# Kernel optimization log

Measured on AMD Instinct MI355X. Metric: run time of the kernel, lower is better.

The kernel has to match this reference:

```python
import jax, jax.numpy as jnp
import numpy as np

T, D, I, E, G, LG, K = 2048, 1024, 512, 32, 8, 4, 6
SI = 2 * I  # shared expert inter dim = n_shared_experts * inter_dim
ROUTE_SCALE = 1.0


def setup_inputs() -> dict:
    key = jax.random.key(0)
    ks = jax.random.split(key, 16)
    s = 0.02
    f = jnp.float32
    return {
        "x": jax.random.normal(ks[0], (T, D), f),
        "router_w": jax.random.normal(ks[1], (E, D), f) * s,
        "router_b": jax.random.normal(ks[2], (E,), f) * s,
        "W1": jax.random.normal(ks[3], (E, D, I), f) * s,
        "b1": jax.random.normal(ks[4], (E, I), f) * s,
        "W2": jax.random.normal(ks[5], (E, D, I), f) * s,
        "b2": jax.random.normal(ks[6], (E, I), f) * s,
        "W3": jax.random.normal(ks[7], (E, I, D), f) * s,
        "b3": jax.random.normal(ks[8], (E, D), f) * s,
        "sw1": jax.random.normal(ks[9], (D, SI), f) * s,
        "sb1": jax.random.normal(ks[10], (SI,), f) * s,
        "sw2": jax.random.normal(ks[11], (D, SI), f) * s,
        "sb2": jax.random.normal(ks[12], (SI,), f) * s,
        "sw3": jax.random.normal(ks[13], (SI, D), f) * s,
        "sb3": jax.random.normal(ks[14], (D,), f) * s,
    }


def _route(x, router_w, router_b):
    # Router: softmax scores (fp32), group-limited top-k.
    logits = x @ router_w.T + router_b                      # [T, E]
    scores = jax.nn.softmax(logits.astype(jnp.float32), axis=-1)
    original = scores
    sg = scores.reshape(x.shape[0], G, E // G)              # [T, G, E/G]
    # no router bias -> group score = sum of top-2 expert scores per group
    group_scores = jnp.sum(jax.lax.top_k(sg, 2)[0], axis=-1)  # [T, G]
    _, gidx = jax.lax.top_k(group_scores, LG)               # [T, LG]
    keep = jnp.zeros((x.shape[0], G), bool).at[jnp.arange(x.shape[0])[:, None], gidx].set(True)
    masked = jnp.where(keep[:, :, None], sg, -jnp.inf).reshape(x.shape[0], E)
    _, idx = jax.lax.top_k(masked, K)                       # [T, K]
    vals = jnp.take_along_axis(original, idx, axis=1) * ROUTE_SCALE
    return vals.astype(x.dtype), idx


def reference(x, router_w, router_b, W1, b1, W2, b2, W3, b3, sw1, sb1, sw2, sb2, sw3, sb3):
    vals, idx = _route(x, router_w, router_b)
    # dense gate matrix [T, E]; top-k indices per row are distinct
    gates = jnp.zeros((x.shape[0], E), x.dtype).at[jnp.arange(x.shape[0])[:, None], idx].set(vals)
    # routed experts: Expert(x) = W3 @ silu(w1(x) * w2(x))
    h1 = jnp.einsum('td,edi->tei', x, W1) + b1              # [T, E, I]
    h2 = jnp.einsum('td,edi->tei', x, W2) + b2
    h = jax.nn.silu(h1 * h2)
    y = jnp.einsum('tei,eid->td', h * gates[:, :, None], W3) + gates @ b3
    # shared expert
    z = jax.nn.silu((x @ sw1 + sb1) * (x @ sw2 + sb2)) @ sw3 + sb3
    return y + z
```

## Files before the change

### kernel.cpp

```cpp
#include <hip/hip_runtime.h>
#include <hip/hip_bf16.h>
#include <math.h>

#define T_CONST 2048
#define D_CONST 1024
#define I_CONST 512
#define SI_CONST 1024
#define E_CONST 32
#define G_CONST 8
#define LG_CONST 4
#define KSEL 6

#define BM 128
#define BN 64
#define BK 64

typedef __attribute__((ext_vector_type(8))) short short8;
typedef __attribute__((ext_vector_type(4))) float floatx4;

__device__ inline unsigned pack_bf16(float a, float b) {
  __hip_bfloat162 h = __float22bfloat162_rn(float2{a, b});
  return *reinterpret_cast<unsigned*>(&h);
}

__device__ inline void gload16(const void* g, void* l) {
  __builtin_amdgcn_global_load_lds(
      (const __attribute__((address_space(1))) unsigned int*)g,
      (__attribute__((address_space(3))) unsigned int*)l, 16, 0, 0);
}

__global__ __launch_bounds__(256) void cvt_x(const float* __restrict__ in,
                                             __hip_bfloat16* __restrict__ out) {
  size_t i = ((size_t)blockIdx.x * 256 + threadIdx.x) * 4;
  float4 v = *(const float4*)&in[i];
  uint2 u{pack_bf16(v.x, v.y), pack_bf16(v.z, v.w)};
  *(uint2*)&out[i] = u;
}

__global__ __launch_bounds__(256) void cvt_rwt(const float* __restrict__ rw,
                                               float* __restrict__ rwt) {
  int i = blockIdx.x * 256 + threadIdx.x;
  int d = i >> 5, e = i & 31;
  rwt[d * 32 + e] = rw[e * D_CONST + d];
}

__global__ __launch_bounds__(256) void transpose_all(
    const float* __restrict__ W1, const float* __restrict__ W2,
    const float* __restrict__ W3, const float* __restrict__ sw1,
    const float* __restrict__ sw2, const float* __restrict__ sw3,
    __hip_bfloat16* __restrict__ W1t, __hip_bfloat16* __restrict__ W2t,
    __hip_bfloat16* __restrict__ W3t, __hip_bfloat16* __restrict__ sw1t,
    __hip_bfloat16* __restrict__ sw2t, __hip_bfloat16* __restrict__ sw3t) {
  __shared__ float tile[64][65];
  int b = blockIdx.x;
  const float* in;
  __hip_bfloat16* out;
  int K, N, k0, n0;
  if (b < 8192) {
    int local = b & 4095;
    int mat = local >> 7, rem = local & 127;
    K = 1024; N = 512;
    in = ((b < 4096) ? W1 : W2) + (size_t)mat * (1024 * 512);
    out = ((b < 4096) ? W1t : W2t) + (size_t)mat * (1024 * 512);
    n0 = (rem & 7) * 64; k0 = (rem >> 3) * 64;
  } else if (b < 12288) {
    int local = b - 8192;
    int mat = local >> 7, rem = local & 127;
    K = 512; N = 1024;
    in = W3 + (size_t)mat * (512 * 1024);
    out = W3t + (size_t)mat * (512 * 1024);
    n0 = (rem & 15) * 64; k0 = (rem >> 4) * 64;
  } else {
    int local = b - 12288;
    int which = local >> 8, rem = local & 255;
    K = 1024; N = 1024;
    in = which == 0 ? sw1 : which == 1 ? sw2 : sw3;
    out = which == 0 ? sw1t : which == 1 ? sw2t : sw3t;
    n0 = (rem & 15) * 64; k0 = (rem >> 4) * 64;
  }
  int tid = threadIdx.x;
  int tr = tid >> 4, tc4 = (tid & 15) * 4;
#pragma unroll
  for (int i = 0; i < 4; ++i) {
    float4 v = *(const float4*)&in[(size_t)(k0 + tr + 16 * i) * N + n0 + tc4];
    tile[tr + 16 * i][tc4 + 0] = v.x;
    tile[tr + 16 * i][tc4 + 1] = v.y;
    tile[tr + 16 * i][tc4 + 2] = v.z;
    tile[tr + 16 * i][tc4 + 3] = v.w;
  }
  __syncthreads();
#pragma unroll
  for (int i = 0; i < 4; ++i) {
    int n = tr + 16 * i;
    unsigned lo = pack_bf16(tile[tc4 + 0][n], tile[tc4 + 1][n]);
    unsigned hi = pack_bf16(tile[tc4 + 2][n], tile[tc4 + 3][n]);
    uint2 u{lo, hi};
    *(uint2*)&out[(size_t)(n0 + n) * K + k0 + tc4] = u;
  }
}

__global__ __launch_bounds__(256) void router2(
    const float* __restrict__ x, const float* __restrict__ rwt,
    const float* __restrict__ rb, int* __restrict__ counts,
    int* __restrict__ slots, float* __restrict__ gatel) {
  const int lane = threadIdx.x & 63;
  const int wv = threadIdx.x >> 6;
  const int t = blockIdx.x * 4 + wv;
  const int e = lane & 31, h = lane >> 5;
  const float* xp = x + (size_t)t * D_CONST;
  float s = 0.f;
#pragma unroll 8
  for (int d = h; d < D_CONST; d += 2) s = fmaf(xp[d], rwt[d * 32 + e], s);
  s += __shfl_xor(s, 32);
  s += rb[e];
  float mx = s;
#pragma unroll
  for (int m = 16; m >= 1; m >>= 1) mx = fmaxf(mx, __shfl_xor(mx, m));
  float p = expf(s - mx);
  float sum = p;
#pragma unroll
  for (int m = 16; m >= 1; m >>= 1) sum += __shfl_xor(sum, m);
  float sc = p / sum;
  float a = sc, bb = __shfl_xor(a, 1);
  float hi = fmaxf(a, bb), lo = fminf(a, bb);
  float oh = __shfl_xor(hi, 2), ol = __shfl_xor(lo, 2);
  float gs = fmaxf(fmaxf(hi + oh, hi + lo), oh + ol);
  const int g = e >> 2;
  unsigned keep = 0;
  float gv = gs;
#pragma unroll
  for (int r = 0; r < LG_CONST; ++r) {
    float v = gv;
    int gi = g;
#pragma unroll
    for (int m = 16; m >= 1; m >>= 1) {
      float ov = __shfl_xor(v, m);
      int og = __shfl_xor(gi, m);
      if (ov > v || (ov == v && og < gi)) { v = ov; gi = og; }
    }
    keep |= 1u << gi;
    if (g == gi) gv = -1e30f;
  }
  float cand = ((keep >> g) & 1u) ? sc : -1e30f;
  int sel_e = -1;
  float sel_v = 0.f;
#pragma unroll
  for (int r = 0; r < KSEL; ++r) {
    float v = cand;
    int ei = e;
#pragma unroll
    for (int m = 16; m >= 1; m >>= 1) {
      float ov = __shfl_xor(v, m);
      int oe = __shfl_xor(ei, m);
      if (ov > v || (ov == v && oe < ei)) { v = ov; ei = oe; }
    }
    if (lane == r) { sel_e = ei; sel_v = v; }
    if (e == ei) cand = -1e30f;
  }
  if (lane < KSEL) {
    int pos = atomicAdd(&counts[sel_e], 1);
    slots[sel_e * T_CONST + pos] = t * KSEL + lane;
    gatel[sel_e * T_CONST + pos] = sel_v;
  }
}

template <bool GATHER>
__global__ __launch_bounds__(256, 2) void up_mfma2(
    const __hip_bfloat16* __restrict__ Abf, const __hip_bfloat16* __restrict__ B1t,
    const __hip_bfloat16* __restrict__ B2t, const float* __restrict__ bias1,
    const float* __restrict__ bias2, const int* __restrict__ counts,
    const int* __restrict__ slots, __hip_bfloat16* __restrict__ Hout,
    int N, int Kd) {
  const int e = GATHER ? blockIdx.z : 0;
  const int cnt = GATHER ? counts[e] : T_CONST;
  const int m0 = blockIdx.y * BM;
  if (m0 >= cnt) return;
  const int n0 = blockIdx.x * BN;

  __shared__ short As[8 * BM * 8];
  __shared__ short Bs1[8 * BN * 8];
  __shared__ short Bs2[8 * BN * 8];
  __shared__ int srow[BM];
  __shared__ int sdst[BM];

  const int tid = threadIdx.x;
  const int lane = tid & 63, wv = tid >> 6;
  if (tid < BM) {
    int r = m0 + tid;
    bool valid = r < cnt;
    if (GATHER) {
      int sl = valid ? slots[e * T_CONST + r] : 0;
      srow[tid] = valid ? sl / KSEL : 0;
      sdst[tid] = valid ? sl : -1;
    } else {
      srow[tid] = valid ? r : 0;
      sdst[tid] = valid ? r : -1;
    }
  }
  __syncthreads();

  const char* agp[4];
  short* alds[4];
  const char* bgp[4];
  short* blds[4];
  {
    int row0 = srow[lane], row1 = srow[64 + lane];
#pragma unroll
    for (int i = 0; i < 4; ++i) {
      int kc = 2 * wv + (i >> 1);
      int mh = i & 1;
      agp[i] = (const char*)(Abf + (size_t)(mh ? row1 : row0) * Kd + kc * 8);
      alds[i] = (short*)As + (kc * BM + mh * 64 + lane) * 8;
    }
    const __hip_bfloat16* Bsel = (wv < 2 ? B1t : B2t) + (size_t)e * N * Kd;
    short* Lsel = (wv < 2) ? (short*)Bs1 : (short*)Bs2;
    int wl = wv & 1;
#pragma unroll
    for (int i = 0; i < 4; ++i) {
      int kc = wl * 4 + i;
      bgp[i] = (const char*)(Bsel + (size_t)(n0 + lane) * Kd + kc * 8);
      blds[i] = Lsel + (kc * BN + lane) * 8;
    }
  }

  const int l15 = lane & 15, quad = lane >> 4;
  const int wm = wv & 1, wn = wv >> 1;
  floatx4 acc1[4][2] = {};
  floatx4 acc2[4][2] = {};
  const int kiter = Kd / BK;

  for (int it = 0; it < kiter; ++it) {
#pragma unroll
    for (int i = 0; i < 4; ++i) gload16(agp[i], alds[i]);
#pragma unroll
    for (int i = 0; i < 4; ++i) gload16(bgp[i], blds[i]);
#pragma unroll
    for (int i = 0; i < 4; ++i) { agp[i] += BK * 2; bgp[i] += BK * 2; }
    __syncthreads();
    short8 a[2][4];
#pragma unroll
    for (int s = 0; s < 2; ++s)
#pragma unroll
      for (int mi = 0; mi < 4; ++mi)
        a[s][mi] = *(const short8*)&As[((s * 4 + quad) * BM + wm * 64 + mi * 16 + l15) * 8];
#pragma unroll
    for (int s = 0; s < 2; ++s)
#pragma unroll
      for (int ni = 0; ni < 2; ++ni) {
        short8 b1 = *(const short8*)&Bs1[((s * 4 + quad) * BN + wn * 32 + ni * 16 + l15) * 8];
        short8 b2 = *(const short8*)&Bs2[((s * 4 + quad) * BN + wn * 32 + ni * 16 + l15) * 8];
#pragma unroll
        for (int mi = 0; mi < 4; ++mi) {
          acc1[mi][ni] = __builtin_amdgcn_mfma_f32_16x16x32_bf16(a[s][mi], b1, acc1[mi][ni], 0, 0, 0);
          acc2[mi][ni] = __builtin_amdgcn_mfma_f32_16x16x32_bf16(a[s][mi], b2, acc2[mi][ni], 0, 0, 0);
        }
      }
    __syncthreads();
  }

  const float* bb1 = bias1 + (size_t)e * N + n0;
  const float* bb2 = bias2 + (size_t)e * N + n0;
#pragma unroll
  for (int mi = 0; mi < 4; ++mi) {
#pragma unroll
    for (int ni = 0; ni < 2; ++ni) {
      int n = wn * 32 + ni * 16 + l15;
      float c1 = bb1[n], c2 = bb2[n];
#pragma unroll
      for (int reg = 0; reg < 4; ++reg) {
        int row = wm * 64 + mi * 16 + quad * 4 + reg;
        int dst = sdst[row];
        if (dst < 0) continue;
        float h1 = acc1[mi][ni][reg] + c1;
        float h2 = acc2[mi][ni][reg] + c2;
        float p = h1 * h2;
        float sv = p / (1.f + expf(-p));
        Hout[(size_t)dst * N + n0 + n] = __float2bfloat16(sv);
      }
    }
  }
}

template <bool ROUTED>
__global__ __launch_bounds__(256, 2) void down_mfma2(
    const __hip_bfloat16* __restrict__ Hin, const __hip_bfloat16* __restrict__ Bt,
    const float* __restrict__ bd, const int* __restrict__ counts,
    const int* __restrict__ slots, const float* __restrict__ gatel,
    float* __restrict__ Out, int Kd) {
  const int e = ROUTED ? blockIdx.z : 0;
  const int cnt = ROUTED ? counts[e] : T_CONST;
  const int m0 = blockIdx.y * BM;
  if (m0 >= cnt) return;
  const int n0 = blockIdx.x * BN;

  __shared__ short As[8 * BM * 8];
  __shared__ short Bs[8 * BN * 8];
  __shared__ int ssrc[BM];
  __shared__ int stok[BM];
  __shared__ float sg[BM];

  const int tid = threadIdx.x;
  const int lane = tid & 63, wv = tid >> 6;
  if (tid < BM) {
    int r = m0 + tid;
    bool valid = r < cnt;
    if (ROUTED) {
      int sl = valid ? slots[e * T_CONST + r] : 0;
      ssrc[tid] = sl;
      stok[tid] = valid ? (sl / KSEL) : -1;
      sg[tid] = valid ? gatel[e * T_CONST + r] : 0.f;
    } else {
      ssrc[tid] = valid ? r : 0;
      stok[tid] = valid ? r : -1;
      sg[tid] = 1.f;
    }
  }
  __syncthreads();

  const char* agp[4];
  short* alds[4];
  const char* bgp[2];
  short* blds[2];
  {
    int row0 = ssrc[lane], row1 = ssrc[64 + lane];
#pragma unroll
    for (int i = 0; i < 4; ++i) {
      int kc = 2 * wv + (i >> 1);
      int mh = i & 1;
      agp[i] = (const char*)(Hin + (size_t)(mh ? row1 : row0) * Kd + kc * 8);
      alds[i] = (short*)As + (kc * BM + mh * 64 + lane) * 8;
    }
    const __hip_bfloat16* Bsel = Bt + (size_t)e * D_CONST * Kd;
#pragma unroll
    for (int i = 0; i < 2; ++i) {
      int kc = 2 * wv + i;
      bgp[i] = (const char*)(Bsel + (size_t)(n0 + lane) * Kd + kc * 8);
      blds[i] = (short*)Bs + (kc * BN + lane) * 8;
    }
  }

  const int l15 = lane & 15, quad = lane >> 4;
  const int wm = wv & 1, wn = wv >> 1;
  floatx4 acc[4][2] = {};
  const int kiter = Kd / BK;

  for (int it = 0; it < kiter; ++it) {
#pragma unroll
    for (int i = 0; i < 4; ++i) gload16(agp[i], alds[i]);
#pragma unroll
    for (int i = 0; i < 2; ++i) gload16(bgp[i], blds[i]);
#pragma unroll
    for (int i = 0; i < 4; ++i) agp[i] += BK * 2;
#pragma unroll
    for (int i = 0; i < 2; ++i) bgp[i] += BK * 2;
    __syncthreads();
    short8 a[2][4];
#pragma unroll
    for (int s = 0; s < 2; ++s)
#pragma unroll
      for (int mi = 0; mi < 4; ++mi)
        a[s][mi] = *(const short8*)&As[((s * 4 + quad) * BM + wm * 64 + mi * 16 + l15) * 8];
#pragma unroll
    for (int s = 0; s < 2; ++s)
#pragma unroll
      for (int ni = 0; ni < 2; ++ni) {
        short8 b = *(const short8*)&Bs[((s * 4 + quad) * BN + wn * 32 + ni * 16 + l15) * 8];
#pragma unroll
        for (int mi = 0; mi < 4; ++mi)
          acc[mi][ni] = __builtin_amdgcn_mfma_f32_16x16x32_bf16(a[s][mi], b, acc[mi][ni], 0, 0, 0);
      }
    __syncthreads();
  }

#pragma unroll
  for (int mi = 0; mi < 4; ++mi) {
#pragma unroll
    for (int ni = 0; ni < 2; ++ni) {
      int n = n0 + wn * 32 + ni * 16 + l15;
      float bias = ROUTED ? bd[(size_t)e * D_CONST + n] : bd[n];
#pragma unroll
      for (int reg = 0; reg < 4; ++reg) {
        int row = wm * 64 + mi * 16 + quad * 4 + reg;
        int tok = stok[row];
        if (tok < 0) continue;
        if (ROUTED) {
          float v = sg[row] * (acc[mi][ni][reg] + bias);
          atomicAdd(&Out[(size_t)tok * D_CONST + n], v);
        } else {
          Out[(size_t)tok * D_CONST + n] = acc[mi][ni][reg] + bias;
        }
      }
    }
  }
}

extern "C" void kernel_launch(void* const* d_in, const int* in_sizes, int n_in,
                              void* d_out, int out_size, void* d_ws, size_t ws_size,
                              hipStream_t stream) {
  const float* x   = (const float*)d_in[0];
  const float* rw  = (const float*)d_in[1];
  const float* rb  = (const float*)d_in[2];
  const float* W1  = (const float*)d_in[3];
  const float* b1  = (const float*)d_in[4];
  const float* W2  = (const float*)d_in[5];
  const float* b2  = (const float*)d_in[6];
  const float* W3  = (const float*)d_in[7];
  const float* b3  = (const float*)d_in[8];
  const float* sw1 = (const float*)d_in[9];
  const float* sb1 = (const float*)d_in[10];
  const float* sw2 = (const float*)d_in[11];
  const float* sb2 = (const float*)d_in[12];
  const float* sw3 = (const float*)d_in[13];
  const float* sb3 = (const float*)d_in[14];
  float* out = (float*)d_out;

  char* w = (char*)d_ws;
  size_t off = 0;
  auto alloc = [&](size_t bytes) {
    char* p = w + off;
    off += (bytes + 255) & ~(size_t)255;
    return p;
  };
  int* counts = (int*)alloc(E_CONST * 4);
  int* slots = (int*)alloc((size_t)E_CONST * T_CONST * 4);
  float* gatel = (float*)alloc((size_t)E_CONST * T_CONST * 4);
  float* rwt = (float*)alloc((size_t)D_CONST * E_CONST * 4);
  __hip_bfloat16* x_bf = (__hip_bfloat16*)alloc((size_t)T_CONST * D_CONST * 2);
  __hip_bfloat16* W1t = (__hip_bfloat16*)alloc((size_t)E_CONST * D_CONST * I_CONST * 2);
  __hip_bfloat16* W2t = (__hip_bfloat16*)alloc((size_t)E_CONST * D_CONST * I_CONST * 2);
  __hip_bfloat16* W3t = (__hip_bfloat16*)alloc((size_t)E_CONST * I_CONST * D_CONST * 2);
  __hip_bfloat16* sw1t = (__hip_bfloat16*)alloc((size_t)D_CONST * SI_CONST * 2);
  __hip_bfloat16* sw2t = (__hip_bfloat16*)alloc((size_t)D_CONST * SI_CONST * 2);
  __hip_bfloat16* sw3t = (__hip_bfloat16*)alloc((size_t)SI_CONST * D_CONST * 2);
  __hip_bfloat16* Hbuf = (__hip_bfloat16*)alloc((size_t)T_CONST * KSEL * I_CONST * 2);
  __hip_bfloat16* Hs = (__hip_bfloat16*)alloc((size_t)T_CONST * SI_CONST * 2);

  hipMemsetAsync(counts, 0, E_CONST * sizeof(int), stream);
  cvt_rwt<<<(D_CONST * E_CONST) / 256, 256, 0, stream>>>(rw, rwt);
  cvt_x<<<(T_CONST * D_CONST) / 1024, 256, 0, stream>>>(x, x_bf);
  transpose_all<<<13056, 256, 0, stream>>>(W1, W2, W3, sw1, sw2, sw3,
                                           W1t, W2t, W3t, sw1t, sw2t, sw3t);
  router2<<<T_CONST / 4, 256, 0, stream>>>(x, rwt, rb, counts, slots, gatel);
  up_mfma2<true><<<dim3(I_CONST / BN, T_CONST / BM, E_CONST), 256, 0, stream>>>(
      x_bf, W1t, W2t, b1, b2, counts, slots, Hbuf, I_CONST, D_CONST);
  up_mfma2<false><<<dim3(SI_CONST / BN, T_CONST / BM, 1), 256, 0, stream>>>(
      x_bf, sw1t, sw2t, sb1, sb2, nullptr, nullptr, Hs, SI_CONST, D_CONST);
  down_mfma2<false><<<dim3(D_CONST / BN, T_CONST / BM, 1), 256, 0, stream>>>(
      Hs, sw3t, sb3, nullptr, nullptr, nullptr, out, SI_CONST);
  down_mfma2<true><<<dim3(D_CONST / BN, T_CONST / BM, E_CONST), 256, 0, stream>>>(
      Hbuf, W3t, b3, counts, slots, gatel, out, I_CONST);
}
```

Measured before the change: 537.7 us.

## Gather routed tokens contiguously and fuse shared/routed expert GEMMs with larger swizzled tiles

Router now records token ids per expert, a scan builds per-expert offsets, and a gather kernel copies routed token rows of x into a contiguous buffer. The up and down projections for routed and shared experts each run in one launch, with the shared expert as an extra z-slice. Tiles grow from 128x64 to 128x128 and LDS uses an XOR swizzle to cut bank conflicts. This removes launches and indirect row loads inside the GEMMs and raises per-block reuse. In exchange it adds a gather pass, a single-thread scan, an output memset, and atomic adds for the shared expert output too.

```diff
diff --git a/kernel.cpp b/kernel.cpp
--- a/kernel.cpp
+++ b/kernel.cpp
@@ -10,10 +10,6 @@
 #define G_CONST 8
 #define LG_CONST 4
 #define KSEL 6
-
-#define BM 128
-#define BN 64
-#define BK 64
 
 typedef __attribute__((ext_vector_type(8))) short short8;
 typedef __attribute__((ext_vector_type(4))) float floatx4;
@@ -102,7 +98,7 @@
 __global__ __launch_bounds__(256) void router2(
     const float* __restrict__ x, const float* __restrict__ rwt,
     const float* __restrict__ rb, int* __restrict__ counts,
-    int* __restrict__ slots, float* __restrict__ gatel) {
+    int* __restrict__ stok, float* __restrict__ gatel) {
   const int lane = threadIdx.x & 63;
   const int wv = threadIdx.x >> 6;
   const int t = blockIdx.x * 4 + wv;
@@ -159,236 +155,242 @@
   }
   if (lane < KSEL) {
     int pos = atomicAdd(&counts[sel_e], 1);
-    slots[sel_e * T_CONST + pos] = t * KSEL + lane;
+    stok[sel_e * T_CONST + pos] = t;
     gatel[sel_e * T_CONST + pos] = sel_v;
   }
 }
 
-template <bool GATHER>
-__global__ __launch_bounds__(256, 2) void up_mfma2(
-    const __hip_bfloat16* __restrict__ Abf, const __hip_bfloat16* __restrict__ B1t,
-    const __hip_bfloat16* __restrict__ B2t, const float* __restrict__ bias1,
-    const float* __restrict__ bias2, const int* __restrict__ counts,
-    const int* __restrict__ slots, __hip_bfloat16* __restrict__ Hout,
-    int N, int Kd) {
-  const int e = GATHER ? blockIdx.z : 0;
-  const int cnt = GATHER ? counts[e] : T_CONST;
-  const int m0 = blockIdx.y * BM;
+__global__ void scan_k(const int* __restrict__ counts, int* __restrict__ offsets) {
+  if (threadIdx.x == 0) {
+    int s = 0;
+    for (int e = 0; e < E_CONST; ++e) { offsets[e] = s; s += counts[e]; }
+    offsets[E_CONST] = s;
+  }
+}
+
+__global__ __launch_bounds__(256) void gather_x(
+    const __hip_bfloat16* __restrict__ xbf, const int* __restrict__ counts,
+    const int* __restrict__ offsets, const int* __restrict__ stok,
+    const float* __restrict__ gatel, __hip_bfloat16* __restrict__ Xg,
+    int* __restrict__ ctok, float* __restrict__ cgate) {
+  int e = blockIdx.x;
+  int cnt = counts[e];
+  int row = blockIdx.y * 16 + (threadIdx.x >> 4);
+  if (row >= cnt) return;
+  int seg = threadIdx.x & 15;
+  int tok = stok[e * T_CONST + row];
+  int dst = offsets[e] + row;
+  const uint4* src = (const uint4*)(xbf + (size_t)tok * D_CONST);
+  uint4* d = (uint4*)(Xg + (size_t)dst * D_CONST);
+#pragma unroll
+  for (int i = 0; i < 8; ++i) d[i * 16 + seg] = src[i * 16 + seg];
+  if (seg == 0) { ctok[dst] = tok; cgate[dst] = gatel[e * T_CONST + row]; }
+}
+
+__global__ __launch_bounds__(256, 2) void up_fused(
+    const __hip_bfloat16* __restrict__ Xg, const __hip_bfloat16* __restrict__ xbf,
+    const __hip_bfloat16* __restrict__ W1t, const __hip_bfloat16* __restrict__ W2t,
+    const __hip_bfloat16* __restrict__ sw1t, const __hip_bfloat16* __restrict__ sw2t,
+    const float* __restrict__ b1, const float* __restrict__ b2,
+    const float* __restrict__ sb1, const float* __restrict__ sb2,
+    const int* __restrict__ counts, const int* __restrict__ offsets,
+    __hip_bfloat16* __restrict__ He, __hip_bfloat16* __restrict__ Hs) {
+  const int z = blockIdx.z;
+  const bool SH = (z == E_CONST);
+  const int N = SH ? SI_CONST : I_CONST;
+  const int n0 = blockIdx.x * 128;
+  if (n0 >= N) return;
+  const int cnt = SH ? T_CONST : counts[z];
+  const int m0 = blockIdx.y * 128;
   if (m0 >= cnt) return;
-  const int n0 = blockIdx.x * BN;
-
-  __shared__ short As[8 * BM * 8];
-  __shared__ short Bs1[8 * BN * 8];
-  __shared__ short Bs2[8 * BN * 8];
-  __shared__ int srow[BM];
-  __shared__ int sdst[BM];
-
-  const int tid = threadIdx.x;
-  const int lane = tid & 63, wv = tid >> 6;
-  if (tid < BM) {
-    int r = m0 + tid;
-    bool valid = r < cnt;
-    if (GATHER) {
-      int sl = valid ? slots[e * T_CONST + r] : 0;
-      srow[tid] = valid ? sl / KSEL : 0;
-      sdst[tid] = valid ? sl : -1;
-    } else {
-      srow[tid] = valid ? r : 0;
-      sdst[tid] = valid ? r : -1;
-    }
-  }
-  __syncthreads();
-
-  const char* agp[4];
-  short* alds[4];
-  const char* bgp[4];
-  short* blds[4];
-  {
-    int row0 = srow[lane], row1 = srow[64 + lane];
-#pragma unroll
-    for (int i = 0; i < 4; ++i) {
-      int kc = 2 * wv + (i >> 1);
-      int mh = i & 1;
-      agp[i] = (const char*)(Abf + (size_t)(mh ? row1 : row0) * Kd + kc * 8);
-      alds[i] = (short*)As + (kc * BM + mh * 64 + lane) * 8;
-    }
-    const __hip_bfloat16* Bsel = (wv < 2 ? B1t : B2t) + (size_t)e * N * Kd;
-    short* Lsel = (wv < 2) ? (short*)Bs1 : (short*)Bs2;
-    int wl = wv & 1;
-#pragma unroll
-    for (int i = 0; i < 4; ++i) {
-      int kc = wl * 4 + i;
-      bgp[i] = (const char*)(Bsel + (size_t)(n0 + lane) * Kd + kc * 8);
-      blds[i] = Lsel + (kc * BN + lane) * 8;
-    }
-  }
-
+  const int base = SH ? 0 : offsets[z];
+
+  const __hip_bfloat16* Ab = SH ? (xbf + (size_t)m0 * D_CONST)
+                                : (Xg + (size_t)(base + m0) * D_CONST);
+  const __hip_bfloat16* B1 = SH ? (sw1t + (size_t)n0 * D_CONST)
+                                : (W1t + ((size_t)z * I_CONST + n0) * D_CONST);
+  const __hip_bfloat16* B2 = SH ? (sw2t + (size_t)n0 * D_CONST)
+                                : (W2t + ((size_t)z * I_CONST + n0) * D_CONST);
+
+  __shared__ short As[8192], Bs1[8192], Bs2[8192];
+
+  const int tid = threadIdx.x, lane = tid & 63, wv = tid >> 6;
   const int l15 = lane & 15, quad = lane >> 4;
   const int wm = wv & 1, wn = wv >> 1;
-  floatx4 acc1[4][2] = {};
-  floatx4 acc2[4][2] = {};
-  const int kiter = Kd / BK;
-
-  for (int it = 0; it < kiter; ++it) {
-#pragma unroll
-    for (int i = 0; i < 4; ++i) gload16(agp[i], alds[i]);
-#pragma unroll
-    for (int i = 0; i < 4; ++i) gload16(bgp[i], blds[i]);
-#pragma unroll
-    for (int i = 0; i < 4; ++i) { agp[i] += BK * 2; bgp[i] += BK * 2; }
+  const int lr = lane >> 3, lc = lane & 7, kap = lc ^ lr;
+
+  const __hip_bfloat16 *aG[4], *b1G[4], *b2G[4];
+#pragma unroll
+  for (int i = 0; i < 4; ++i) {
+    int r = (wv * 4 + i) * 8 + lr;
+    aG[i] = Ab + (size_t)r * D_CONST + kap * 8;
+    b1G[i] = B1 + (size_t)r * D_CONST + kap * 8;
+    b2G[i] = B2 + (size_t)r * D_CONST + kap * 8;
+  }
+  const int ldsu = (wv * 4 * 64 + lane) * 8;
+
+  floatx4 acc1[4][4] = {};
+  floatx4 acc2[4][4] = {};
+
+  for (int it = 0; it < D_CONST / 64; ++it) {
+#pragma unroll
+    for (int i = 0; i < 4; ++i) {
+      gload16(aG[i], &As[ldsu + i * 512]);
+      gload16(b1G[i], &Bs1[ldsu + i * 512]);
+      gload16(b2G[i], &Bs2[ldsu + i * 512]);
+      aG[i] += 64; b1G[i] += 64; b2G[i] += 64;
+    }
     __syncthreads();
-    short8 a[2][4];
-#pragma unroll
-    for (int s = 0; s < 2; ++s)
+#pragma unroll
+    for (int c = 0; c < 2; ++c) {
+      const int kc = c * 4 + quad;
+      short8 a[4], x1[4], x2[4];
+#pragma unroll
+      for (int mi = 0; mi < 4; ++mi) {
+        int m = wm * 64 + mi * 16 + l15;
+        a[mi] = *(const short8*)&As[(m * 8 + (kc ^ (m & 7))) * 8];
+      }
+#pragma unroll
+      for (int ni = 0; ni < 4; ++ni) {
+        int n = wn * 64 + ni * 16 + l15;
+        int u = (n * 8 + (kc ^ (n & 7))) * 8;
+        x1[ni] = *(const short8*)&Bs1[u];
+        x2[ni] = *(const short8*)&Bs2[u];
+      }
 #pragma unroll
       for (int mi = 0; mi < 4; ++mi)
-        a[s][mi] = *(const short8*)&As[((s * 4 + quad) * BM + wm * 64 + mi * 16 + l15) * 8];
-#pragma unroll
-    for (int s = 0; s < 2; ++s)
-#pragma unroll
-      for (int ni = 0; ni < 2; ++ni) {
-        short8 b1 = *(const short8*)&Bs1[((s * 4 + quad) * BN + wn * 32 + ni * 16 + l15) * 8];
-        short8 b2 = *(const short8*)&Bs2[((s * 4 + quad) * BN + wn * 32 + ni * 16 + l15) * 8];
-#pragma unroll
-        for (int mi = 0; mi < 4; ++mi) {
-          acc1[mi][ni] = __builtin_amdgcn_mfma_f32_16x16x32_bf16(a[s][mi], b1, acc1[mi][ni], 0, 0, 0);
-          acc2[mi][ni] = __builtin_amdgcn_mfma_f32_16x16x32_bf16(a[s][mi], b2, acc2[mi][ni], 0, 0, 0);
+#pragma unroll
+        for (int ni = 0; ni < 4; ++ni) {
+          acc1[mi][ni] = __builtin_amdgcn_mfma_f32_16x16x32_bf16(a[mi], x1[ni], acc1[mi][ni], 0, 0, 0);
+          acc2[mi][ni] = __builtin_amdgcn_mfma_f32_16x16x32_bf16(a[mi], x2[ni], acc2[mi][ni], 0, 0, 0);
         }
-      }
+    }
     __syncthreads();
   }
 
-  const float* bb1 = bias1 + (size_t)e * N + n0;
-  const float* bb2 = bias2 + (size_t)e * N + n0;
+  const float* pb1 = SH ? sb1 : (b1 + (size_t)z * I_CONST);
+  const float* pb2 = SH ? sb2 : (b2 + (size_t)z * I_CONST);
+  __hip_bfloat16* outp = SH ? (Hs + (size_t)m0 * SI_CONST + n0)
+                            : (He + (size_t)(base + m0) * I_CONST + n0);
+  const int ldo = SH ? SI_CONST : I_CONST;
+  float c1[4], c2[4];
+#pragma unroll
+  for (int ni = 0; ni < 4; ++ni) {
+    int n = wn * 64 + ni * 16 + l15;
+    c1[ni] = pb1[n0 + n];
+    c2[ni] = pb2[n0 + n];
+  }
 #pragma unroll
   for (int mi = 0; mi < 4; ++mi) {
 #pragma unroll
-    for (int ni = 0; ni < 2; ++ni) {
-      int n = wn * 32 + ni * 16 + l15;
-      float c1 = bb1[n], c2 = bb2[n];
-#pragma unroll
-      for (int reg = 0; reg < 4; ++reg) {
-        int row = wm * 64 + mi * 16 + quad * 4 + reg;
-        int dst = sdst[row];
-        if (dst < 0) continue;
-        float h1 = acc1[mi][ni][reg] + c1;
-        float h2 = acc2[mi][ni][reg] + c2;
+    for (int reg = 0; reg < 4; ++reg) {
+      int m = wm * 64 + mi * 16 + quad * 4 + reg;
+      if (m0 + m >= cnt) continue;
+#pragma unroll
+      for (int ni = 0; ni < 4; ++ni) {
+        int n = wn * 64 + ni * 16 + l15;
+        float h1 = acc1[mi][ni][reg] + c1[ni];
+        float h2 = acc2[mi][ni][reg] + c2[ni];
         float p = h1 * h2;
-        float sv = p / (1.f + expf(-p));
-        Hout[(size_t)dst * N + n0 + n] = __float2bfloat16(sv);
-      }
-    }
-  }
-}
-
-template <bool ROUTED>
-__global__ __launch_bounds__(256, 2) void down_mfma2(
-    const __hip_bfloat16* __restrict__ Hin, const __hip_bfloat16* __restrict__ Bt,
-    const float* __restrict__ bd, const int* __restrict__ counts,
-    const int* __restrict__ slots, const float* __restrict__ gatel,
-    float* __restrict__ Out, int Kd) {
-  const int e = ROUTED ? blockIdx.z : 0;
-  const int cnt = ROUTED ? counts[e] : T_CONST;
-  const int m0 = blockIdx.y * BM;
+        float s = p / (1.f + expf(-p));
+        outp[(size_t)m * ldo + n] = __float2bfloat16(s);
+      }
+    }
+  }
+}
+
+__global__ __launch_bounds__(256, 3) void down_fused(
+    const __hip_bfloat16* __restrict__ He, const __hip_bfloat16* __restrict__ Hs,
+    const __hip_bfloat16* __restrict__ W3t, const __hip_bfloat16* __restrict__ sw3t,
+    const float* __restrict__ b3, const float* __restrict__ sb3,
+    const int* __restrict__ counts, const int* __restrict__ offsets,
+    const int* __restrict__ ctok, const float* __restrict__ cgate,
+    float* __restrict__ out) {
+  const int z = blockIdx.z;
+  const bool SH = (z == E_CONST);
+  const int n0 = blockIdx.x * 128;
+  const int cnt = SH ? T_CONST : counts[z];
+  const int m0 = blockIdx.y * 128;
   if (m0 >= cnt) return;
-  const int n0 = blockIdx.x * BN;
-
-  __shared__ short As[8 * BM * 8];
-  __shared__ short Bs[8 * BN * 8];
-  __shared__ int ssrc[BM];
-  __shared__ int stok[BM];
-  __shared__ float sg[BM];
-
-  const int tid = threadIdx.x;
-  const int lane = tid & 63, wv = tid >> 6;
-  if (tid < BM) {
-    int r = m0 + tid;
-    bool valid = r < cnt;
-    if (ROUTED) {
-      int sl = valid ? slots[e * T_CONST + r] : 0;
-      ssrc[tid] = sl;
-      stok[tid] = valid ? (sl / KSEL) : -1;
-      sg[tid] = valid ? gatel[e * T_CONST + r] : 0.f;
-    } else {
-      ssrc[tid] = valid ? r : 0;
-      stok[tid] = valid ? r : -1;
-      sg[tid] = 1.f;
-    }
-  }
-  __syncthreads();
-
-  const char* agp[4];
-  short* alds[4];
-  const char* bgp[2];
-  short* blds[2];
-  {
-    int row0 = ssrc[lane], row1 = ssrc[64 + lane];
-#pragma unroll
-    for (int i = 0; i < 4; ++i) {
-      int kc = 2 * wv + (i >> 1);
-      int mh = i & 1;
-      agp[i] = (const char*)(Hin + (size_t)(mh ? row1 : row0) * Kd + kc * 8);
-      alds[i] = (short*)As + (kc * BM + mh * 64 + lane) * 8;
-    }
-    const __hip_bfloat16* Bsel = Bt + (size_t)e * D_CONST * Kd;
-#pragma unroll
-    for (int i = 0; i < 2; ++i) {
-      int kc = 2 * wv + i;
-      bgp[i] = (const char*)(Bsel + (size_t)(n0 + lane) * Kd + kc * 8);
-      blds[i] = (short*)Bs + (kc * BN + lane) * 8;
-    }
-  }
-
+  const int base = SH ? 0 : offsets[z];
+  const int Kd = SH ? SI_CONST : I_CONST;
+
+  const __hip_bfloat16* Ab = SH ? (Hs + (size_t)m0 * SI_CONST)
+                                : (He + (size_t)(base + m0) * I_CONST);
+  const __hip_bfloat16* Bb = SH ? (sw3t + (size_t)n0 * SI_CONST)
+                                : (W3t + ((size_t)z * D_CONST + n0) * I_CONST);
+
+  __shared__ short As[8192], Bs[8192];
+
+  const int tid = threadIdx.x, lane = tid & 63, wv = tid >> 6;
   const int l15 = lane & 15, quad = lane >> 4;
   const int wm = wv & 1, wn = wv >> 1;
-  floatx4 acc[4][2] = {};
-  const int kiter = Kd / BK;
+  const int lr = lane >> 3, lc = lane & 7, kap = lc ^ lr;
+
+  const __hip_bfloat16 *aG[4], *bG[4];
+#pragma unroll
+  for (int i = 0; i < 4; ++i) {
+    int r = (wv * 4 + i) * 8 + lr;
+    aG[i] = Ab + (size_t)r * Kd + kap * 8;
+    bG[i] = Bb + (size_t)r * Kd + kap * 8;
+  }
+  const int ldsu = (wv * 4 * 64 + lane) * 8;
+
+  floatx4 acc[4][4] = {};
+  const int kiter = Kd / 64;
 
   for (int it = 0; it < kiter; ++it) {
 #pragma unroll
-    for (int i = 0; i < 4; ++i) gload16(agp[i], alds[i]);
-#pragma unroll
-    for (int i = 0; i < 2; ++i) gload16(bgp[i], blds[i]);
-#pragma unroll
-    for (int i = 0; i < 4; ++i) agp[i] += BK * 2;
-#pragma unroll
-    for (int i = 0; i < 2; ++i) bgp[i] += BK * 2;
+    for (int i = 0; i < 4; ++i) {
+      gload16(aG[i], &As[ldsu + i * 512]);
+      gload16(bG[i], &Bs[ldsu + i * 512]);
+      aG[i] += 64; bG[i] += 64;
+    }
     __syncthreads();
-    short8 a[2][4];
-#pragma unroll
-    for (int s = 0; s < 2; ++s)
+#pragma unroll
+    for (int c = 0; c < 2; ++c) {
+      const int kc = c * 4 + quad;
+      short8 a[4], bbf[4];
+#pragma unroll
+      for (int mi = 0; mi < 4; ++mi) {
+        int m = wm * 64 + mi * 16 + l15;
+        a[mi] = *(const short8*)&As[(m * 8 + (kc ^ (m & 7))) * 8];
+      }
+#pragma unroll
+      for (int ni = 0; ni < 4; ++ni) {
+        int n = wn * 64 + ni * 16 + l15;
+        bbf[ni] = *(const short8*)&Bs[(n * 8 + (kc ^ (n & 7))) * 8];
+      }
 #pragma unroll
       for (int mi = 0; mi < 4; ++mi)
-        a[s][mi] = *(const short8*)&As[((s * 4 + quad) * BM + wm * 64 + mi * 16 + l15) * 8];
-#pragma unroll
-    for (int s = 0; s < 2; ++s)
-#pragma unroll
-      for (int ni = 0; ni < 2; ++ni) {
-        short8 b = *(const short8*)&Bs[((s * 4 + quad) * BN + wn * 32 + ni * 16 + l15) * 8];
-#pragma unroll
-        for (int mi = 0; mi < 4; ++mi)
-          acc[mi][ni] = __builtin_amdgcn_mfma_f32_16x16x32_bf16(a[s][mi], b, acc[mi][ni], 0, 0, 0);
-      }
+#pragma unroll
+        for (int ni = 0; ni < 4; ++ni)
+          acc[mi][ni] = __builtin_amdgcn_mfma_f32_16x16x32_bf16(a[mi], bbf[ni], acc[mi][ni], 0, 0, 0);
+    }
     __syncthreads();
   }
 
+  float bias[4];
+#pragma unroll
+  for (int ni = 0; ni < 4; ++ni) {
+    int n = n0 + wn * 64 + ni * 16 + l15;
+    bias[ni] = SH ? sb3[n] : b3[(size_t)z * D_CONST + n];
+  }
 #pragma unroll
   for (int mi = 0; mi < 4; ++mi) {
 #pragma unroll
-    for (int ni = 0; ni < 2; ++ni) {
-      int n = n0 + wn * 32 + ni * 16 + l15;
-      float bias = ROUTED ? bd[(size_t)e * D_CONST + n] : bd[n];
-#pragma unroll
-      for (int reg = 0; reg < 4; ++reg) {
-        int row = wm * 64 + mi * 16 + quad * 4 + reg;
-        int tok = stok[row];
-        if (tok < 0) continue;
-        if (ROUTED) {
-          float v = sg[row] * (acc[mi][ni][reg] + bias);
-          atomicAdd(&Out[(size_t)tok * D_CONST + n], v);
-        } else {
-          Out[(size_t)tok * D_CONST + n] = acc[mi][ni][reg] + bias;
-        }
+    for (int reg = 0; reg < 4; ++reg) {
+      int m = wm * 64 + mi * 16 + quad * 4 + reg;
+      if (m0 + m >= cnt) continue;
+      int tok;
+      float gate;
+      if (SH) { tok = m0 + m; gate = 1.f; }
+      else { int grow = base + m0 + m; tok = ctok[grow]; gate = cgate[grow]; }
+#pragma unroll
+      for (int ni = 0; ni < 4; ++ni) {
+        int n = n0 + wn * 64 + ni * 16 + l15;
+        float v = gate * (acc[mi][ni][reg] + bias[ni]);
+        atomicAdd(&out[(size_t)tok * D_CONST + n], v);
       }
     }
   }
@@ -422,31 +424,35 @@
     return p;
   };
   int* counts = (int*)alloc(E_CONST * 4);
-  int* slots = (int*)alloc((size_t)E_CONST * T_CONST * 4);
+  int* offsets = (int*)alloc((E_CONST + 1) * 4);
+  int* stok = (int*)alloc((size_t)E_CONST * T_CONST * 4);
   float* gatel = (float*)alloc((size_t)E_CONST * T_CONST * 4);
   float* rwt = (float*)alloc((size_t)D_CONST * E_CONST * 4);
+  int* ctok = (int*)alloc((size_t)T_CONST * KSEL * 4);
+  float* cgate = (float*)alloc((size_t)T_CONST * KSEL * 4);
   __hip_bfloat16* x_bf = (__hip_bfloat16*)alloc((size_t)T_CONST * D_CONST * 2);
+  __hip_bfloat16* Xg = (__hip_bfloat16*)alloc((size_t)(T_CONST * KSEL + 128) * D_CONST * 2);
   __hip_bfloat16* W1t = (__hip_bfloat16*)alloc((size_t)E_CONST * D_CONST * I_CONST * 2);
   __hip_bfloat16* W2t = (__hip_bfloat16*)alloc((size_t)E_CONST * D_CONST * I_CONST * 2);
   __hip_bfloat16* W3t = (__hip_bfloat16*)alloc((size_t)E_CONST * I_CONST * D_CONST * 2);
   __hip_bfloat16* sw1t = (__hip_bfloat16*)alloc((size_t)D_CONST * SI_CONST * 2);
   __hip_bfloat16* sw2t = (__hip_bfloat16*)alloc((size_t)D_CONST * SI_CONST * 2);
   __hip_bfloat16* sw3t = (__hip_bfloat16*)alloc((size_t)SI_CONST * D_CONST * 2);
-  __hip_bfloat16* Hbuf = (__hip_bfloat16*)alloc((size_t)T_CONST * KSEL * I_CONST * 2);
+  __hip_bfloat16* He = (__hip_bfloat16*)alloc((size_t)(T_CONST * KSEL + 128) * I_CONST * 2);
   __hip_bfloat16* Hs = (__hip_bfloat16*)alloc((size_t)T_CONST * SI_CONST * 2);
 
   hipMemsetAsync(counts, 0, E_CONST * sizeof(int), stream);
+  hipMemsetAsync(out, 0, (size_t)out_size * sizeof(float), stream);
   cvt_rwt<<<(D_CONST * E_CONST) / 256, 256, 0, stream>>>(rw, rwt);
   cvt_x<<<(T_CONST * D_CONST) / 1024, 256, 0, stream>>>(x, x_bf);
   transpose_all<<<13056, 256, 0, stream>>>(W1, W2, W3, sw1, sw2, sw3,
                                            W1t, W2t, W3t, sw1t, sw2t, sw3t);
-  router2<<<T_CONST / 4, 256, 0, stream>>>(x, rwt, rb, counts, slots, gatel);
-  up_mfma2<true><<<dim3(I_CONST / BN, T_CONST / BM, E_CONST), 256, 0, stream>>>(
-      x_bf, W1t, W2t, b1, b2, counts, slots, Hbuf, I_CONST, D_CONST);
-  up_mfma2<false><<<dim3(SI_CONST / BN, T_CONST / BM, 1), 256, 0, stream>>>(
-      x_bf, sw1t, sw2t, sb1, sb2, nullptr, nullptr, Hs, SI_CONST, D_CONST);
-  down_mfma2<false><<<dim3(D_CONST / BN, T_CONST / BM, 1), 256, 0, stream>>>(
-      Hs, sw3t, sb3, nullptr, nullptr, nullptr, out, SI_CONST);
-  down_mfma2<true><<<dim3(D_CONST / BN, T_CONST / BM, E_CONST), 256, 0, stream>>>(
-      Hbuf, W3t, b3, counts, slots, gatel, out, I_CONST);
-}
+  router2<<<T_CONST / 4, 256, 0, stream>>>(x, rwt, rb, counts, stok, gatel);
+  scan_k<<<1, 64, 0, stream>>>(counts, offsets);
+  gather_x<<<dim3(E_CONST, T_CONST / 16), 256, 0, stream>>>(
+      x_bf, counts, offsets, stok, gatel, Xg, ctok, cgate);
+  up_fused<<<dim3(8, 16, E_CONST + 1), 256, 0, stream>>>(
+      Xg, x_bf, W1t, W2t, sw1t, sw2t, b1, b2, sb1, sb2, counts, offsets, He, Hs);
+  down_fused<<<dim3(8, 16, E_CONST + 1), 256, 0, stream>>>(
+      He, Hs, W3t, sw3t, b3, sb3, counts, offsets, ctok, cgate, out);
+}
```

New measurement: 506.3 us. 5.8% less time.
